# Performance work log

Hardware: AMD Instinct MI355X
Metric: run time of the kernel (lower is better)

## Reference

```python
import jax, jax.numpy as jnp
import numpy as np

D_MODEL = 4096
N_EXPERTS = 64
TOP_K = 2


def setup_inputs() -> dict:
    key = jax.random.key(0)
    kx, kw = jax.random.split(key)
    x = jax.random.normal(kx, (4, 8192, D_MODEL), dtype=jnp.float32)
    # nn.Linear(d_model, n_experts, bias=False) weight: [n_experts, d_model]
    W = jax.random.normal(kw, (N_EXPERTS, D_MODEL), dtype=jnp.float32) * (1.0 / np.sqrt(D_MODEL))
    return {"x": x, "W": W}


def reference(x, W):
    # logits: [B, S, n_experts]
    logits = jnp.einsum("bsd,ed->bse", x, W)
    # top-k values and indices along expert dim
    weights, experts = jax.lax.top_k(logits, TOP_K)
    weights = jax.nn.softmax(weights, axis=-1)
    return weights, experts
```

## Files before the change

kernel.cpp:

```cpp
#include <hip/hip_runtime.h>
#include <math.h>

#define D_MODEL 4096
#define N_EXP   64

typedef _Float16 half8 __attribute__((ext_vector_type(8)));
typedef float    f32x4 __attribute__((ext_vector_type(4)));

__global__ __launch_bounds__(256)
void wprep_kernel(const float* __restrict__ W,
                  _Float16* __restrict__ whf, _Float16* __restrict__ wlf) {
    const int gid   = blockIdx.x * 256 + threadIdx.x;
    const int lane  = gid & 63;
    const int ntk   = gid >> 6;
    const int nt    = ntk & 3;
    const int kstep = ntk >> 2;
    const int e  = nt * 16 + (lane & 15);
    const int k0 = kstep * 32 + (lane >> 4) * 8;

    const float* src = W + (size_t)e * D_MODEL + k0;
    float4 w0 = *(const float4*)(src);
    float4 w1 = *(const float4*)(src + 4);
    float wv[8] = {w0.x, w0.y, w0.z, w0.w, w1.x, w1.y, w1.z, w1.w};

    half8 hh, ll;
    #pragma unroll
    for (int j = 0; j < 8; ++j) {
        float ws = wv[j] * 64.0f;
        _Float16 h = (_Float16)ws;
        hh[j] = h;
        ll[j] = (_Float16)((ws - (float)h) * 4096.0f);
    }
    *(half8*)(whf + (size_t)gid * 8) = hh;
    *(half8*)(wlf + (size_t)gid * 8) = ll;
}

#define GLD16(gp, lp) __builtin_amdgcn_global_load_lds( \
    (const __attribute__((address_space(1))) unsigned int*)(const void*)(gp), \
    (__attribute__((address_space(3))) unsigned int*)(void*)(lp), 16, 0, 0)

__device__ __forceinline__ void cvt_hilo(const float4 a, const float4 b,
                                         half8& hi, half8& lo) {
    float av[8] = {a.x, a.y, a.z, a.w, b.x, b.y, b.z, b.w};
    #pragma unroll
    for (int j = 0; j < 8; ++j) {
        _Float16 h = (_Float16)av[j];
        hi[j] = h;
        lo[j] = (_Float16)((av[j] - (float)h) * 4096.0f);
    }
}

__global__ __launch_bounds__(512, 1)
void router_kernel(const float* __restrict__ x,
                   const _Float16* __restrict__ whf,
                   const _Float16* __restrict__ wlf,
                   float* __restrict__ out, int ntok) {
    __shared__ _Float16 sB[2][8][2][4][512];

    const int tid  = threadIdx.x;
    const int w    = tid >> 6;
    const int l    = tid & 63;
    const int tok0 = blockIdx.x * 128;
    const float* ax = x + (size_t)(tok0 + w * 16 + (l & 15)) * D_MODEL + (l >> 4) * 8;

    f32x4 hh[4], cc[4];
    #pragma unroll
    for (int nt = 0; nt < 4; ++nt) { hh[nt] = (f32x4)0.0f; cc[nt] = (f32x4)0.0f; }

    {
        const size_t co = ((size_t)w * 4) * 512 + (size_t)l * 8;
        #pragma unroll
        for (int nt = 0; nt < 4; ++nt) {
            GLD16(whf + co + nt * 512, &sB[0][w][0][nt][0]);
            GLD16(wlf + co + nt * 512, &sB[0][w][1][nt][0]);
        }
    }
    float4 A0a = *(const float4*)(ax + 0 * 32), A0b = *(const float4*)(ax + 0 * 32 + 4);
    float4 A1a = *(const float4*)(ax + 1 * 32), A1b = *(const float4*)(ax + 1 * 32 + 4);
    float4 A2a = *(const float4*)(ax + 2 * 32), A2b = *(const float4*)(ax + 2 * 32 + 4);
    float4 A3a = *(const float4*)(ax + 3 * 32), A3b = *(const float4*)(ax + 3 * 32 + 4);

    __syncthreads();

    for (int g = 0; g < 16; ++g) {
        const int cur = g & 1;
        if (g < 15) {
            const int ksg = (g + 1) * 8 + w;
            const size_t co = ((size_t)ksg * 4) * 512 + (size_t)l * 8;
            #pragma unroll
            for (int nt = 0; nt < 4; ++nt) {
                GLD16(whf + co + nt * 512, &sB[cur ^ 1][w][0][nt][0]);
                GLD16(wlf + co + nt * 512, &sB[cur ^ 1][w][1][nt][0]);
            }
        }

#define STEP(KSL, SA, SB)                                                      \
        {                                                                      \
            const int ks = g * 8 + KSL;                                        \
            half8 ah, al;                                                      \
            cvt_hilo(SA, SB, ah, al);                        \
            const int kp = (ks + 4 < 128) ? (ks + 4) : 127;                    \
            SA = *(const float4*)(ax + (size_t)kp * 32);           \
            SB = *(const float4*)(ax + (size_t)kp * 32 + 4);                   \
            half8 bh[4], bl[4];                                                \
            _Pragma("unroll")                                                  \
            for (int nt = 0; nt < 4; ++nt) {                                   \
                bh[nt] = *(const half8*)&sB[cur][KSL][0][nt][l * 8];           \
                bl[nt] = *(const half8*)&sB[cur][KSL][1][nt][l * 8];           \
            }                                                                  \
            _Pragma("unroll")                                                  \
            for (int nt = 0; nt < 4; ++nt)                                     \
                hh[nt] = __builtin_amdgcn_mfma_f32_16x16x32_f16(ah, bh[nt], hh[nt], 0, 0, 0); \
            _Pragma("unroll")                                                  \
            for (int nt = 0; nt < 4; ++nt)                                     \
                cc[nt] = __builtin_amdgcn_mfma_f32_16x16x32_f16(ah, bl[nt], cc[nt], 0, 0, 0); \
            _Pragma("unroll")                                                  \
            for (int nt = 0; nt < 4; ++nt)                                     \
                cc[nt] = __builtin_amdgcn_mfma_f32_16x16x32_f16(al, bh[nt], cc[nt], 0, 0, 0); \
        }

        STEP(0, A0a, A0b) STEP(1, A1a, A1b) STEP(2, A2a, A2b) STEP(3, A3a, A3b)
        STEP(4, A0a, A0b) STEP(5, A1a, A1b) STEP(6, A2a, A2b) STEP(7, A3a, A3b)
#undef STEP

        __syncthreads();
    }

    float tt[4][4];
    #pragma unroll
    for (int nt = 0; nt < 4; ++nt) {
        f32x4 tot = (hh[nt] + cc[nt] * (1.0f / 4096.0f)) * (1.0f / 64.0f);
        tt[nt][0] = tot.x; tt[nt][1] = tot.y; tt[nt][2] = tot.z; tt[nt][3] = tot.w;
    }

    float* out_e = out + (size_t)2 * ntok;

    #pragma unroll
    for (int q = 0; q < 4; ++q) {
        float v1 = -3.0e38f, v2 = -3.0e38f;
        int   i1 = 1 << 30,  i2 = 1 << 30;
        #pragma unroll
        for (int nt = 0; nt < 4; ++nt) {
            float v  = tt[nt][q];
            int   id = nt * 16 + (l & 15);
            if (v > v1 || (v == v1 && id < i1)) {
                v2 = v1; i2 = i1; v1 = v; i1 = id;
            } else if (v > v2 || (v == v2 && id < i2)) {
                v2 = v; i2 = id;
            }
        }
        #pragma unroll
        for (int m = 1; m < 16; m <<= 1) {
            float ov1 = __shfl_xor(v1, m, 64);
            int   oi1 = __shfl_xor(i1, m, 64);
            float ov2 = __shfl_xor(v2, m, 64);
            int   oi2 = __shfl_xor(i2, m, 64);
            bool ofirst = (ov1 > v1) || (ov1 == v1 && oi1 < i1);
            if (ofirst) {
                bool s2 = (ov2 > v1) || (ov2 == v1 && oi2 < i1);
                v2 = s2 ? ov2 : v1;  i2 = s2 ? oi2 : i1;
                v1 = ov1;            i1 = oi1;
            } else {
                bool s2 = (ov1 > v2) || (ov1 == v2 && oi1 < i2);
                v2 = s2 ? ov1 : v2;  i2 = s2 ? oi1 : i2;
            }
        }

        if ((l & 15) == 0) {
            const int tok = tok0 + w * 16 + (l >> 4) * 4 + q;
            float e = expf(v2 - v1);
            float d = 1.0f + e;
            out[2 * tok + 0] = 1.0f / d;
            out[2 * tok + 1] = e / d;
            out_e[2 * tok + 0] = (float)i1;
            out_e[2 * tok + 1] = (float)i2;
        }
    }
}

extern "C" void kernel_launch(void* const* d_in, const int* in_sizes, int n_in,
                              void* d_out, int out_size, void* d_ws, size_t ws_size,
                              hipStream_t stream) {
    const float* x = (const float*)d_in[0];
    const float* W = (const float*)d_in[1];
    float* out = (float*)d_out;
    const int ntok = in_sizes[0] / D_MODEL;

    _Float16* whf = (_Float16*)d_ws;
    _Float16* wlf = (_Float16*)d_ws + (size_t)N_EXP * D_MODEL;

    wprep_kernel<<<dim3(128), dim3(256), 0, stream>>>(W, whf, wlf);
    router_kernel<<<dim3(ntok / 128), dim3(512), 0, stream>>>(x, whf, wlf, out, ntok);
}
```

Before: 143.2 us.

## Halve router block size and prefetch activations a whole group ahead

```diff
diff --git a/kernel.cpp b/kernel.cpp
--- a/kernel.cpp
+++ b/kernel.cpp
@@ -50,17 +50,17 @@
     }
 }
 
-__global__ __launch_bounds__(512, 1)
+__global__ __launch_bounds__(256, 2)
 void router_kernel(const float* __restrict__ x,
                    const _Float16* __restrict__ whf,
                    const _Float16* __restrict__ wlf,
                    float* __restrict__ out, int ntok) {
-    __shared__ _Float16 sB[2][8][2][4][512];
+    __shared__ _Float16 sB[2][4][2][4][512];
 
     const int tid  = threadIdx.x;
     const int w    = tid >> 6;
     const int l    = tid & 63;
-    const int tok0 = blockIdx.x * 128;
+    const int tok0 = blockIdx.x * 64;
     const float* ax = x + (size_t)(tok0 + w * 16 + (l & 15)) * D_MODEL + (l >> 4) * 8;
 
     f32x4 hh[4], cc[4];
@@ -68,63 +68,84 @@
     for (int nt = 0; nt < 4; ++nt) { hh[nt] = (f32x4)0.0f; cc[nt] = (f32x4)0.0f; }
 
     {
-        const size_t co = ((size_t)w * 4) * 512 + (size_t)l * 8;
+        const size_t co = (size_t)w * 4 * 512 + (size_t)l * 8;
         #pragma unroll
         for (int nt = 0; nt < 4; ++nt) {
             GLD16(whf + co + nt * 512, &sB[0][w][0][nt][0]);
             GLD16(wlf + co + nt * 512, &sB[0][w][1][nt][0]);
         }
     }
-    float4 A0a = *(const float4*)(ax + 0 * 32), A0b = *(const float4*)(ax + 0 * 32 + 4);
-    float4 A1a = *(const float4*)(ax + 1 * 32), A1b = *(const float4*)(ax + 1 * 32 + 4);
-    float4 A2a = *(const float4*)(ax + 2 * 32), A2b = *(const float4*)(ax + 2 * 32 + 4);
-    float4 A3a = *(const float4*)(ax + 3 * 32), A3b = *(const float4*)(ax + 3 * 32 + 4);
+    float4 P0a = *(const float4*)(ax + 0 * 32), P0b = *(const float4*)(ax + 0 * 32 + 4);
+    float4 P1a = *(const float4*)(ax + 1 * 32), P1b = *(const float4*)(ax + 1 * 32 + 4);
+    float4 P2a = *(const float4*)(ax + 2 * 32), P2b = *(const float4*)(ax + 2 * 32 + 4);
+    float4 P3a = *(const float4*)(ax + 3 * 32), P3b = *(const float4*)(ax + 3 * 32 + 4);
+    float4 P4a = *(const float4*)(ax + 4 * 32), P4b = *(const float4*)(ax + 4 * 32 + 4);
+    float4 P5a = *(const float4*)(ax + 5 * 32), P5b = *(const float4*)(ax + 5 * 32 + 4);
+    float4 P6a = *(const float4*)(ax + 6 * 32), P6b = *(const float4*)(ax + 6 * 32 + 4);
+    float4 P7a = *(const float4*)(ax + 7 * 32), P7b = *(const float4*)(ax + 7 * 32 + 4);
 
     __syncthreads();
 
-    for (int g = 0; g < 16; ++g) {
-        const int cur = g & 1;
-        if (g < 15) {
-            const int ksg = (g + 1) * 8 + w;
-            const size_t co = ((size_t)ksg * 4) * 512 + (size_t)l * 8;
-            #pragma unroll
-            for (int nt = 0; nt < 4; ++nt) {
-                GLD16(whf + co + nt * 512, &sB[cur ^ 1][w][0][nt][0]);
-                GLD16(wlf + co + nt * 512, &sB[cur ^ 1][w][1][nt][0]);
-            }
-        }
-
-#define STEP(KSL, SA, SB)                                                      \
-        {                                                                      \
-            const int ks = g * 8 + KSL;                                        \
-            half8 ah, al;                                                      \
-            cvt_hilo(SA, SB, ah, al);                        \
-            const int kp = (ks + 4 < 128) ? (ks + 4) : 127;                    \
-            SA = *(const float4*)(ax + (size_t)kp * 32);           \
-            SB = *(const float4*)(ax + (size_t)kp * 32 + 4);                   \
-            half8 bh[4], bl[4];                                                \
+#define STEP(KSL, SA, SB, CUR)                                                 \
+    {                                                                          \
+        half8 ah, al;                                                          \
+        cvt_hilo(SA, SB, ah, al);                                              \
+        half8 bh[4], bl[4];                                                    \
+        _Pragma("unroll")                                                      \
+        for (int nt = 0; nt < 4; ++nt) {                                       \
+            bh[nt] = *(const half8*)&sB[CUR][KSL][0][nt][l * 8];               \
+            bl[nt] = *(const half8*)&sB[CUR][KSL][1][nt][l * 8];               \
+        }                                                                      \
+        _Pragma("unroll")                                                      \
+        for (int nt = 0; nt < 4; ++nt)                                         \
+            hh[nt] = __builtin_amdgcn_mfma_f32_16x16x32_f16(ah, bh[nt], hh[nt], 0, 0, 0); \
+        _Pragma("unroll")                                                      \
+        for (int nt = 0; nt < 4; ++nt)                                         \
+            cc[nt] = __builtin_amdgcn_mfma_f32_16x16x32_f16(ah, bl[nt], cc[nt], 0, 0, 0); \
+        _Pragma("unroll")                                                      \
+        for (int nt = 0; nt < 4; ++nt)                                         \
+            cc[nt] = __builtin_amdgcn_mfma_f32_16x16x32_f16(al, bh[nt], cc[nt], 0, 0, 0); \
+    }
+
+#define GROUP(G, CUR, C0a,C0b,C1a,C1b,C2a,C2b,C3a,C3b,                         \
+                      O0a,O0b,O1a,O1b,O2a,O2b,O3a,O3b)                         \
+    {                                                                          \
+        if ((G) >= 1 && (G) <= 30) {                                           \
+            const size_t kb = (size_t)((G) + 1) * 4 * 32;                      \
+            O0a = *(const float4*)(ax + kb + 0 * 32);                          \
+            O0b = *(const float4*)(ax + kb + 0 * 32 + 4);                      \
+            O1a = *(const float4*)(ax + kb + 1 * 32);                          \
+            O1b = *(const float4*)(ax + kb + 1 * 32 + 4);                      \
+            O2a = *(const float4*)(ax + kb + 2 * 32);                          \
+            O2b = *(const float4*)(ax + kb + 2 * 32 + 4);                      \
+            O3a = *(const float4*)(ax + kb + 3 * 32);                          \
+            O3b = *(const float4*)(ax + kb + 3 * 32 + 4);                      \
+        }                                                                      \
+        if ((G) < 31) {                                                        \
+            const int ksg = ((G) + 1) * 4 + w;                                 \
+            const size_t co = (size_t)ksg * 4 * 512 + (size_t)l * 8;           \
             _Pragma("unroll")                                                  \
             for (int nt = 0; nt < 4; ++nt) {                                   \
-                bh[nt] = *(const half8*)&sB[cur][KSL][0][nt][l * 8];           \
-                bl[nt] = *(const half8*)&sB[cur][KSL][1][nt][l * 8];           \
+                GLD16(whf + co + nt * 512, &sB[(CUR) ^ 1][w][0][nt][0]);       \
+                GLD16(wlf + co + nt * 512, &sB[(CUR) ^ 1][w][1][nt][0]);       \
             }                                                                  \
-            _Pragma("unroll")                                                  \
-            for (int nt = 0; nt < 4; ++nt)                                     \
-                hh[nt] = __builtin_amdgcn_mfma_f32_16x16x32_f16(ah, bh[nt], hh[nt], 0, 0, 0); \
-            _Pragma("unroll")                                                  \
-            for (int nt = 0; nt < 4; ++nt)                                     \
-                cc[nt] = __builtin_amdgcn_mfma_f32_16x16x32_f16(ah, bl[nt], cc[nt], 0, 0, 0); \
-            _Pragma("unroll")                                                  \
-            for (int nt = 0; nt < 4; ++nt)                                     \
-                cc[nt] = __builtin_amdgcn_mfma_f32_16x16x32_f16(al, bh[nt], cc[nt], 0, 0, 0); \
-        }
-
-        STEP(0, A0a, A0b) STEP(1, A1a, A1b) STEP(2, A2a, A2b) STEP(3, A3a, A3b)
-        STEP(4, A0a, A0b) STEP(5, A1a, A1b) STEP(6, A2a, A2b) STEP(7, A3a, A3b)
+        }                                                                      \
+        STEP(0, C0a, C0b, CUR)                                                 \
+        STEP(1, C1a, C1b, CUR)                                                 \
+        STEP(2, C2a, C2b, CUR)                                                 \
+        STEP(3, C3a, C3b, CUR)                                                 \
+        __syncthreads();                                                       \
+    }
+
+    for (int gg = 0; gg < 16; ++gg) {
+        const int g0 = gg * 2;
+        GROUP(g0,     0, P0a,P0b,P1a,P1b,P2a,P2b,P3a,P3b,
+                         P4a,P4b,P5a,P5b,P6a,P6b,P7a,P7b)
+        GROUP(g0 + 1, 1, P4a,P4b,P5a,P5b,P6a,P6b,P7a,P7b,
+                         P0a,P0b,P1a,P1b,P2a,P2b,P3a,P3b)
+    }
+#undef GROUP
 #undef STEP
-
-        __syncthreads();
-    }
 
     float tt[4][4];
     #pragma unroll
@@ -190,5 +211,5 @@
     _Float16* wlf = (_Float16*)d_ws + (size_t)N_EXP * D_MODEL;
 
     wprep_kernel<<<dim3(128), dim3(256), 0, stream>>>(W, whf, wlf);
-    router_kernel<<<dim3(ntok / 128), dim3(512), 0, stream>>>(x, whf, wlf, out, ntok);
-}
+    router_kernel<<<dim3(ntok / 64), dim3(256), 0, stream>>>(x, whf, wlf, out, ntok);
+}
```

Measured after the change: 129.6 us (median of 2 runs). 1.1x faster.
